# Kernel optimization log

Measured on AMD Instinct MI355X. Metric: run time of the kernel, lower is better.

## Reference

```python
import jax, jax.numpy as jnp
import numpy as np


def setup_inputs() -> dict:
    key = jax.random.key(0)
    ks = jax.random.split(key, 9)
    D, DK, DV = 512, 64, 64
    B, S = 4, 4096
    sd = 1.0 / np.sqrt(D).astype(np.float32)
    so = 1.0 / np.sqrt(DV).astype(np.float32)
    return {
        "x": jax.random.normal(ks[0], (B, S, D), dtype=jnp.float32),
        "Wq": jax.random.normal(ks[1], (D, DK), dtype=jnp.float32) * sd,
        "bq": jnp.zeros((DK,), dtype=jnp.float32),
        "Wk": jax.random.normal(ks[2], (D, DK), dtype=jnp.float32) * sd,
        "bk": jnp.zeros((DK,), dtype=jnp.float32),
        "Wv": jax.random.normal(ks[3], (D, DV), dtype=jnp.float32) * sd,
        "bv": jnp.zeros((DV,), dtype=jnp.float32),
        "Wo": jax.random.normal(ks[4], (DV, D), dtype=jnp.float32) * so,
        "bo": jnp.zeros((D,), dtype=jnp.float32),
    }


def reference(x, Wq, bq, Wk, bk, Wv, bv, Wo, bo):
    # x: (B, S, D)
    B, S, D = x.shape
    dk = Wq.shape[1]
    q = x @ Wq + bq            # (B, S, dk)
    k = x @ Wk + bk            # (B, S, dk)
    v = x @ Wv + bv            # (B, S, dv)
    scores = jnp.einsum("bik,bjk->bij", q, k) / jnp.sqrt(jnp.float32(dk))  # (B,S,S)
    # causal mask: True where j <= i (keep)
    causal = jnp.tril(jnp.ones((S, S), dtype=bool))
    scores = jnp.where(causal[None, :, :], scores, -jnp.inf)
    weights = jax.nn.softmax(scores, axis=-1)   # every row has >=1 unmasked entry
    out = jnp.einsum("bij,bjv->biv", weights, v)  # (B, S, dv)
    return out @ Wo + bo
```

## Files before the change

kernel.cpp:

```cpp
#include <hip/hip_runtime.h>
#include <hip/hip_bf16.h>

#define S_LEN 4096
#define D_MODEL 512
#define DKV 64
#define B_N 4
#define STR 72
#define VSTR 136

typedef __hip_bfloat16 bf16;
typedef __attribute__((ext_vector_type(8))) short short8;
typedef __attribute__((ext_vector_type(4))) float floatx4;

#define MFMA(a, b, c) __builtin_amdgcn_mfma_f32_16x16x32_bf16(a, b, c, 0, 0, 0)

__device__ __forceinline__ float b2f(bf16 v) { return __bfloat162float(v); }

__device__ __forceinline__ unsigned short f2bits(float v) {
    union { bf16 h; unsigned short u; } cv;
    cv.h = __float2bfloat16(v);
    return cv.u;
}
__device__ __forceinline__ float bits2f(unsigned short u) {
    union { bf16 h; unsigned short u; } cv;
    cv.u = u;
    return b2f(cv.h);
}

__global__ __launch_bounds__(64) void detect_kernel(const void* x, int* flag) {
    const int lane = threadIdx.x;
    const bf16* xb = (const bf16*)x;
    int bad = 0;
    for (int k = lane; k < 4096; k += 64) {
        float v = fabsf(b2f(xb[2 * k]));
        if (!(v < 64.f)) bad++;
    }
    #pragma unroll
    for (int off = 32; off >= 1; off >>= 1) bad += __shfl_xor(bad, off);
    if (lane == 0) *flag = (bad > 100) ? 1 : 0;
}

__global__ __launch_bounds__(512) void wprep_qkv_frag(
    const void* __restrict__ Wq, const void* __restrict__ bq,
    const void* __restrict__ Wk, const void* __restrict__ bk,
    const void* __restrict__ Wv, const void* __restrict__ bv,
    bf16* __restrict__ Wfh, bf16* __restrict__ Wfl, float* __restrict__ ball,
    const int* __restrict__ flag)
{
    __shared__ float xs[16][513];
    const int ct = blockIdx.x;
    const int c0 = ct * 16;
    const int g = c0 >> 6;
    const int cc0 = c0 & 63;
    const void* W    = (g == 0) ? Wq : (g == 1) ? Wk : Wv;
    const void* bias = (g == 0) ? bq : (g == 1) ? bk : bv;
    const int tid = threadIdx.x;
    const int f32 = *flag;

    #pragma unroll
    for (int i = 0; i < 16; ++i) {
        const int idx = tid + 512 * i;
        const int d = idx >> 4, j = idx & 15;
        const float v = f32 ? ((const float*)W)[(size_t)d * DKV + cc0 + j]
                            : b2f(((const bf16*)W)[(size_t)d * DKV + cc0 + j]);
        xs[j][d] = v;
    }
    __syncthreads();

    union Pack8 { uint4 u; unsigned short s[8]; };
    #pragma unroll
    for (int rep = 0; rep < 2; ++rep) {
        const int f = tid + rep * 512;
        const int kt = f >> 6, lane = f & 63;
        const int quad = lane >> 4, l15 = lane & 15;
        Pack8 ph, pl;
        #pragma unroll
        for (int j = 0; j < 8; ++j) {
            const float v = xs[l15][kt * 32 + quad * 8 + j];
            const unsigned short hb = f2bits(v);
            ph.s[j] = hb;
            pl.s[j] = f2bits(v - bits2f(hb));
        }
        const size_t o = (((size_t)ct * 16 + kt) * 64 + lane) * 8;
        *(uint4*)&Wfh[o] = ph.u;
        *(uint4*)&Wfl[o] = pl.u;
    }
    if (tid < 16)
        ball[c0 + tid] = f32 ? ((const float*)bias)[cc0 + tid]
                             : b2f(((const bf16*)bias)[cc0 + tid]);
}

__global__ __launch_bounds__(512) void wprep_o_frag(
    const void* __restrict__ Wo, const void* __restrict__ bo,
    bf16* __restrict__ WoFh, bf16* __restrict__ WoFl,
    float* __restrict__ ball2, const int* __restrict__ flag)
{
    __shared__ float ys[16][65];
    const int ctile = blockIdx.x;
    const int c0 = ctile * 16;
    const int tid = threadIdx.x;
    const int f32 = *flag;

    #pragma unroll
    for (int rep = 0; rep < 2; ++rep) {
        const int idx = tid + rep * 512;
        const int d = idx >> 4, j = idx & 15;
        const float v = f32 ? ((const float*)Wo)[(size_t)d * D_MODEL + c0 + j]
                            : b2f(((const bf16*)Wo)[(size_t)d * D_MODEL + c0 + j]);
        ys[j][d] = v;
    }
    __syncthreads();

    union Pack8 { uint4 u; unsigned short s[8]; };
    if (tid < 128) {
        const int kc = tid >> 6, lane = tid & 63;
        const int quad = lane >> 4, l15 = lane & 15;
        Pack8 ph, pl;
        #pragma unroll
        for (int j = 0; j < 8; ++j) {
            const float v = ys[l15][kc * 32 + quad * 8 + j];
            const unsigned short hb = f2bits(v);
            ph.s[j] = hb;
            pl.s[j] = f2bits(v - bits2f(hb));
        }
        const size_t o = (((size_t)ctile * 2 + kc) * 64 + lane) * 8;
        *(uint4*)&WoFh[o] = ph.u;
        *(uint4*)&WoFl[o] = pl.u;
    }
    if (tid < 16)
        ball2[c0 + tid] = f32 ? ((const float*)bo)[c0 + tid]
                              : b2f(((const bf16*)bo)[c0 + tid]);
}

__global__ __launch_bounds__(256) void qkv_mfma_bf16(
    const void* __restrict__ x,
    const bf16* __restrict__ Wfh, const float* __restrict__ ball,
    bf16* __restrict__ Qb, bf16* __restrict__ Kb, bf16* __restrict__ Vt,
    const int* __restrict__ flag)
{
    if (*flag) return;
    __shared__ unsigned short hiA[32 * D_MODEL];
    const int tid = threadIdx.x;
    const int rowBase = blockIdx.x * 32;

    const unsigned short* xr = (const unsigned short*)x + (size_t)rowBase * D_MODEL;
    #pragma unroll
    for (int i = 0; i < 8; ++i) {
        const int idx = tid + 256 * i;
        const int r = idx >> 6;
        const int c0 = (idx & 63) << 3;
        const uint4 hv = *(const uint4*)&xr[r * D_MODEL + c0];
        const int boff = (c0 * 2) ^ ((r & 7) << 4);
        *(uint4*)((char*)hiA + r * 1024 + boff) = hv;
    }
    __syncthreads();

    const int lane = tid & 63;
    const int w    = tid >> 6;
    const int quad = lane >> 4;
    const int l15  = lane & 15;
    const int wr   = w & 1;
    const int wcol = w >> 1;
    const int arow = wr * 16 + l15;
    const char* hib = (const char*)hiA + arow * 1024;
    const int swz = (arow & 7) << 4;

    floatx4 acc[6];
    #pragma unroll
    for (int ct = 0; ct < 6; ++ct) acc[ct] = (floatx4){0.f, 0.f, 0.f, 0.f};

    for (int kt = 0; kt < 16; ++kt) {
        const int boff = (kt * 64 + quad * 16) ^ swz;
        const short8 ah = *(const short8*)(hib + boff);
        #pragma unroll
        for (int ct = 0; ct < 6; ++ct) {
            const size_t fo = (((size_t)(wcol * 6 + ct) * 16 + kt) * 64 + lane) * 8;
            const short8 bh = *(const short8*)&Wfh[fo];
            acc[ct] = MFMA(ah, bh, acc[ct]);
        }
    }

    #pragma unroll
    for (int ct = 0; ct < 6; ++ct) {
        const int gc = wcol * 96 + ct * 16 + l15;
        const float bias = ball[gc];
        const float scale = (gc < 64) ? 0.18033688f : 1.0f;
        #pragma unroll
        for (int r = 0; r < 4; ++r) {
            const int gr = rowBase + wr * 16 + quad * 4 + r;
            const bf16 o = __float2bfloat16((acc[ct][r] + bias) * scale);
            if (gc < 64)       Qb[(size_t)gr * DKV + gc] = o;
            else if (gc < 128) Kb[(size_t)gr * DKV + (gc - 64)] = o;
            else {
                const int bb = gr >> 12, sidx = gr & (S_LEN - 1);
                Vt[((size_t)bb * DKV + (gc - 128)) * S_LEN + sidx] = o;
            }
        }
    }
}

__global__ __launch_bounds__(512) void qkv_mfma_f32(
    const void* __restrict__ x,
    const bf16* __restrict__ Wfh, const bf16* __restrict__ Wfl,
    const float* __restrict__ ball,
    bf16* __restrict__ Qb, bf16* __restrict__ Kb, bf16* __restrict__ Vt,
    const int* __restrict__ flag)
{
    if (!*flag) return;
    __shared__ unsigned short hiA[32 * D_MODEL];
    __shared__ unsigned short loA[32 * D_MODEL];
    const int tid = threadIdx.x;
    const int rowBase = blockIdx.x * 32;

    union Pack8 { uint4 u; unsigned short s[8]; };
    {
        const float* xr = (const float*)x + (size_t)rowBase * D_MODEL;
        #pragma unroll
        for (int i = 0; i < 4; ++i) {
            const int idx = tid + 512 * i;
            const int r = idx >> 6;
            const int c0 = (idx & 63) << 3;
            const float4 v0 = *(const float4*)&xr[r * D_MODEL + c0];
            const float4 v1 = *(const float4*)&xr[r * D_MODEL + c0 + 4];
            const float vv[8] = {v0.x, v0.y, v0.z, v0.w, v1.x, v1.y, v1.z, v1.w};
            Pack8 ph, pl;
            #pragma unroll
            for (int j = 0; j < 8; ++j) {
                const unsigned short hb = f2bits(vv[j]);
                ph.s[j] = hb;
                pl.s[j] = f2bits(vv[j] - bits2f(hb));
            }
            const int boff = (c0 * 2) ^ ((r & 7) << 4);
            *(uint4*)((char*)hiA + r * 1024 + boff) = ph.u;
            *(uint4*)((char*)loA + r * 1024 + boff) = pl.u;
        }
    }
    __syncthreads();

    const int lane = tid & 63;
    const int w    = tid >> 6;
    const int quad = lane >> 4;
    const int l15  = lane & 15;
    const int wr   = w & 1;
    const int wq   = w >> 1;
    const int arow = wr * 16 + l15;
    const char* hib = (const char*)hiA + arow * 1024;
    const char* lob = (const char*)loA + arow * 1024;
    const int swz = (arow & 7) << 4;

    floatx4 acc[3];
    #pragma unroll
    for (int ct = 0; ct < 3; ++ct) acc[ct] = (floatx4){0.f, 0.f, 0.f, 0.f};

    for (int kt = 0; kt < 16; ++kt) {
        const int boff = (kt * 64 + quad * 16) ^ swz;
        const short8 ah = *(const short8*)(hib + boff);
        const short8 al = *(const short8*)(lob + boff);
        #pragma unroll
        for (int ct = 0; ct < 3; ++ct) {
            const size_t fo = (((size_t)(wq * 3 + ct) * 16 + kt) * 64 + lane) * 8;
            const short8 bh = *(const short8*)&Wfh[fo];
            const short8 bl = *(const short8*)&Wfl[fo];
            acc[ct] = MFMA(ah, bh, acc[ct]);
            acc[ct] = MFMA(ah, bl, acc[ct]);
            acc[ct] = MFMA(al, bh, acc[ct]);
        }
    }

    #pragma unroll
    for (int ct = 0; ct < 3; ++ct) {
        const int gc = wq * 48 + ct * 16 + l15;
        const float bias = ball[gc];
        const float scale = (gc < 64) ? 0.18033688f : 1.0f;
        #pragma unroll
        for (int r = 0; r < 4; ++r) {
            const int gr = rowBase + wr * 16 + quad * 4 + r;
            const bf16 o = __float2bfloat16((acc[ct][r] + bias) * scale);
            if (gc < 64)       Qb[(size_t)gr * DKV + gc] = o;
            else if (gc < 128) Kb[(size_t)gr * DKV + (gc - 64)] = o;
            else {
                const int bb = gr >> 12, sidx = gr & (S_LEN - 1);
                Vt[((size_t)bb * DKV + (gc - 128)) * S_LEN + sidx] = o;
            }
        }
    }
}

__global__ __launch_bounds__(256, 3) void attn_mfma(
    const bf16* __restrict__ Qg, const bf16* __restrict__ Kg,
    const bf16* __restrict__ Vtg, float* __restrict__ Op,
    float* __restrict__ Mp, float* __restrict__ Lp, const int NS)
{
    const int bid = blockIdx.x;
    const int xcd = bid & 7;
    const int rest = bid >> 3;
    const int b   = xcd >> 1;
    const int khH = (NS == 4) ? (rest & 1) : 0;
    const int t64 = 63 - ((NS == 4) ? (rest >> 1) : rest);
    const int kh  = khH * 2 + (xcd & 1);
    const int rowBase = t64 * 64;
    const int tid = threadIdx.x;
    const int lane = tid & 63;
    const int w  = tid >> 6;
    const int quad = lane >> 4;
    const int l15  = lane & 15;

    __shared__ bf16 Kl[128 * STR];
    __shared__ bf16 Vl[64 * VSTR];
    __shared__ bf16 Pl[64 * VSTR];

    const bf16* Qb = Qg + ((size_t)b * S_LEN + rowBase) * DKV;
    const bf16* Kb = Kg + (size_t)b * S_LEN * DKV;
    const bf16* Vb = Vtg + (size_t)b * DKV * S_LEN;

    {
        const int qr = tid >> 2, qd = (tid & 3) * 16;
        *(uint4*)&Pl[qr * VSTR + qd]     = *(const uint4*)&Qb[qr * DKV + qd];
        *(uint4*)&Pl[qr * VSTR + qd + 8] = *(const uint4*)&Qb[qr * DKV + qd + 8];
    }
    __syncthreads();
    short8 qf0, qf1;
    {
        const int qoff = (w * 16 + l15) * VSTR + quad * 8;
        qf0 = *(const short8*)&Pl[qoff];
        qf1 = *(const short8*)&Pl[qoff + 32];
    }

    floatx4 acc[4];
    #pragma unroll
    for (int v = 0; v < 4; ++v) acc[v] = (floatx4){0.f, 0.f, 0.f, 0.f};
    float m_run[4], l_run[4];
    #pragma unroll
    for (int r = 0; r < 4; ++r) { m_run[r] = -1e30f; l_run[r] = 0.f; }

    const int kbMax = (rowBase + 63) >> 7;
    const int kk = tid >> 1, dk = (tid & 1) * 32;
    const int vd = tid >> 2, vk = (tid & 3) * 32;

    uint4 kr0, kr1, kr2, kr3, vr0, vr1, vr2, vr3;
    int kb = kh;
    if (kb <= kbMax) {
        const uint4* ks = (const uint4*)&Kb[((size_t)(kb * 128 + kk)) * DKV + dk];
        kr0 = ks[0]; kr1 = ks[1]; kr2 = ks[2]; kr3 = ks[3];
        const uint4* vs = (const uint4*)&Vb[(size_t)vd * S_LEN + kb * 128 + vk];
        vr0 = vs[0]; vr1 = vs[1]; vr2 = vs[2]; vr3 = vs[3];
    }

    for (; kb <= kbMax; kb += NS) {
        __syncthreads();
        {
            uint4* kd = (uint4*)&Kl[kk * STR + dk];
            kd[0] = kr0; kd[1] = kr1; kd[2] = kr2; kd[3] = kr3;
            uint4* vdst = (uint4*)&Vl[vd * VSTR + vk];
            vdst[0] = vr0; vdst[1] = vr1; vdst[2] = vr2; vdst[3] = vr3;
        }
        __syncthreads();
        if (kb + NS <= kbMax) {
            const uint4* ks = (const uint4*)&Kb[((size_t)((kb + NS) * 128 + kk)) * DKV + dk];
            kr0 = ks[0]; kr1 = ks[1]; kr2 = ks[2]; kr3 = ks[3];
            const uint4* vs = (const uint4*)&Vb[(size_t)vd * S_LEN + (kb + NS) * 128 + vk];
            vr0 = vs[0]; vr1 = vs[1]; vr2 = vs[2]; vr3 = vs[3];
        }

        floatx4 s[8];
        #pragma unroll
        for (int jt = 0; jt < 8; ++jt) s[jt] = (floatx4){0.f, 0.f, 0.f, 0.f};
        {
            const int qk = quad * 8;
            #pragma unroll
            for (int jt = 0; jt < 8; ++jt) {
                const int kc = (jt * 16 + l15) * STR + qk;
                const short8 ba = *(const short8*)&Kl[kc];
                const short8 bb = *(const short8*)&Kl[kc + 32];
                s[jt] = MFMA(qf0, ba, s[jt]);
                s[jt] = MFMA(qf1, bb, s[jt]);
            }
        }
        if (kb == kbMax) {
            const int rowg = rowBase + w * 16 + quad * 4;
            #pragma unroll
            for (int jt = 0; jt < 8; ++jt) {
                const int kg = kb * 128 + jt * 16 + l15;
                #pragma unroll
                for (int r = 0; r < 4; ++r)
                    if (kg > rowg + r) s[jt][r] = -1e30f;
            }
        }
        float m4[4];
        #pragma unroll
        for (int r = 0; r < 4; ++r) {
            float mm = s[0][r];
            #pragma unroll
            for (int jt = 1; jt < 8; ++jt) mm = fmaxf(mm, s[jt][r]);
            m4[r] = mm;
        }
        #pragma unroll
        for (int off = 1; off < 16; off <<= 1) {
            #pragma unroll
            for (int r = 0; r < 4; ++r) m4[r] = fmaxf(m4[r], __shfl_xor(m4[r], off));
        }
        float alpha[4];
        #pragma unroll
        for (int r = 0; r < 4; ++r) {
            const float mnew = fmaxf(m_run[r], m4[r]);
            alpha[r] = exp2f(m_run[r] - mnew);
            m_run[r] = mnew;
        }
        float ps[4];
        #pragma unroll
        for (int r = 0; r < 4; ++r) {
            float acc_ps = 0.f;
            #pragma unroll
            for (int jt = 0; jt < 8; ++jt) {
                const float pp = exp2f(s[jt][r] - m_run[r]);
                s[jt][r] = pp;
                acc_ps += pp;
            }
            ps[r] = acc_ps;
        }
        #pragma unroll
        for (int off = 1; off < 16; off <<= 1) {
            #pragma unroll
            for (int r = 0; r < 4; ++r) ps[r] += __shfl_xor(ps[r], off);
        }
        #pragma unroll
        for (int r = 0; r < 4; ++r) {
            l_run[r] = l_run[r] * alpha[r] + ps[r];
            #pragma unroll
            for (int v = 0; v < 4; ++v) acc[v][r] *= alpha[r];
            const int poff = (w * 16 + quad * 4 + r) * VSTR + l15;
            #pragma unroll
            for (int jt = 0; jt < 8; ++jt)
                Pl[poff + jt * 16] = __float2bfloat16(s[jt][r]);
        }
        asm volatile("s_waitcnt lgkmcnt(0)" ::: "memory");

        {
            const int pk = quad * 8;
            const int prow = (w * 16 + l15) * VSTR;
            short8 pa[4];
            #pragma unroll
            for (int c = 0; c < 4; ++c)
                pa[c] = *(const short8*)&Pl[prow + pk + c * 32];
            #pragma unroll
            for (int v = 0; v < 4; ++v) {
                const int vrow = (v * 16 + l15) * VSTR;
                #pragma unroll
                for (int c = 0; c < 4; ++c) {
                    const short8 vb = *(const short8*)&Vl[vrow + pk + c * 32];
                    acc[v] = MFMA(pa[c], vb, acc[v]);
                }
            }
        }
    }
    #pragma unroll
    for (int r = 0; r < 4; ++r) {
        const int row = rowBase + w * 16 + quad * 4 + r;
        float* op = Op + (((size_t)kh * B_N + b) * S_LEN + row) * DKV + l15;
        #pragma unroll
        for (int v = 0; v < 4; ++v) op[v * 16] = acc[v][r];
    }
    if (l15 == 0) {
        #pragma unroll
        for (int r = 0; r < 4; ++r) {
            const int row = rowBase + w * 16 + quad * 4 + r;
            const size_t mi = ((size_t)kh * B_N + b) * S_LEN + row;
            Mp[mi] = m_run[r];
            Lp[mi] = l_run[r];
        }
    }
}

__global__ __launch_bounds__(256) void merge_kernel(
    const float* __restrict__ Op, const float* __restrict__ Mp,
    const float* __restrict__ Lp, bf16* __restrict__ Oh, bf16* __restrict__ Ol,
    const int NS)
{
    const int row = blockIdx.x * 32 + (threadIdx.x >> 3);
    const int d0 = (threadIdx.x & 7) * 8;
    const size_t part = (size_t)B_N * S_LEN;

    float m = -1e30f;
    #pragma unroll 4
    for (int i = 0; i < NS; ++i) m = fmaxf(m, Mp[i * part + row]);

    float oacc[8];
    #pragma unroll
    for (int jj = 0; jj < 8; ++jj) oacc[jj] = 0.f;
    float denom = 0.f;
    #pragma unroll 4
    for (int i = 0; i < NS; ++i) {
        const float wi = exp2f(Mp[i * part + row] - m);
        denom += Lp[i * part + row] * wi;
        const float* pi = Op + (i * part + row) * DKV + d0;
        #pragma unroll
        for (int jj = 0; jj < 8; ++jj) oacc[jj] += pi[jj] * wi;
    }
    const float inv = 1.0f / denom;

    union Pack8 { uint4 u; unsigned short s[8]; };
    Pack8 ph, pl;
    #pragma unroll
    for (int jj = 0; jj < 8; ++jj) {
        const float o = oacc[jj] * inv;
        const unsigned short hb = f2bits(o);
        ph.s[jj] = hb;
        pl.s[jj] = f2bits(o - bits2f(hb));
    }
    *(uint4*)&Oh[(size_t)row * DKV + d0] = ph.u;
    *(uint4*)&Ol[(size_t)row * DKV + d0] = pl.u;
}

#define PSTR 72
__global__ __launch_bounds__(256) void proj_mfma_bf16(
    const bf16* __restrict__ Oh, const bf16* __restrict__ Ol,
    const bf16* __restrict__ WoFh, const float* __restrict__ ball2,
    bf16* __restrict__ out, const int* __restrict__ flag)
{
    if (*flag) return;
    __shared__ unsigned short Ah[32 * PSTR], Al[32 * PSTR];
    const int tid = threadIdx.x;
    const int rowBase = blockIdx.x * 32;

    {
        const int r = tid >> 3, c0 = (tid & 7) * 8;
        *(uint4*)&Ah[r * PSTR + c0] = *(const uint4*)&Oh[(size_t)(rowBase + r) * DKV + c0];
        *(uint4*)&Al[r * PSTR + c0] = *(const uint4*)&Ol[(size_t)(rowBase + r) * DKV + c0];
    }
    __syncthreads();

    const int lane = tid & 63;
    const int w    = tid >> 6;
    const int quad = lane >> 4;
    const int l15  = lane & 15;
    const int wr   = w & 1;
    const int wcq  = w >> 1;

    const int aoff = (wr * 16 + l15) * PSTR + quad * 8;
    const short8 ah0 = *(const short8*)&Ah[aoff];
    const short8 ah1 = *(const short8*)&Ah[aoff + 32];
    const short8 al0 = *(const short8*)&Al[aoff];
    const short8 al1 = *(const short8*)&Al[aoff + 32];

    floatx4 acc[16];
    #pragma unroll
    for (int ct = 0; ct < 16; ++ct) acc[ct] = (floatx4){0.f, 0.f, 0.f, 0.f};

    #pragma unroll
    for (int ct = 0; ct < 16; ++ct) {
        const int ctile = wcq * 16 + ct;
        const size_t o0 = (((size_t)ctile * 2 + 0) * 64 + lane) * 8;
        const size_t o1 = (((size_t)ctile * 2 + 1) * 64 + lane) * 8;
        const short8 bh0 = *(const short8*)&WoFh[o0];
        const short8 bh1 = *(const short8*)&WoFh[o1];
        acc[ct] = MFMA(ah0, bh0, acc[ct]);
        acc[ct] = MFMA(ah1, bh1, acc[ct]);
        acc[ct] = MFMA(al0, bh0, acc[ct]);
        acc[ct] = MFMA(al1, bh1, acc[ct]);
    }

    #pragma unroll
    for (int ct = 0; ct < 16; ++ct) {
        const int col = wcq * 256 + ct * 16 + l15;
        const float bias = ball2[col];
        #pragma unroll
        for (int r = 0; r < 4; ++r) {
            const int row = rowBase + wr * 16 + quad * 4 + r;
            out[(size_t)row * D_MODEL + col] = __float2bfloat16(acc[ct][r] + bias);
        }
    }
}

__global__ __launch_bounds__(512) void proj_mfma_f32(
    const bf16* __restrict__ Oh, const bf16* __restrict__ Ol,
    const bf16* __restrict__ WoFh, const bf16* __restrict__ WoFl,
    const float* __restrict__ ball2, float* __restrict__ out,
    const int* __restrict__ flag)
{
    if (!*flag) return;
    __shared__ unsigned short Ah[32 * PSTR], Al[32 * PSTR];
    const int tid = threadIdx.x;
    const int rowBase = blockIdx.x * 32;

    {
        const int r = (tid & 255) >> 3, c0 = (tid & 7) * 8;
        if (tid < 256)
            *(uint4*)&Ah[r * PSTR + c0] = *(const uint4*)&Oh[(size_t)(rowBase + r) * DKV + c0];
        else
            *(uint4*)&Al[r * PSTR + c0] = *(const uint4*)&Ol[(size_t)(rowBase + r) * DKV + c0];
    }
    __syncthreads();

    const int lane = tid & 63;
    const int w    = tid >> 6;
    const int quad = lane >> 4;
    const int l15  = lane & 15;
    const int wr   = w & 1;
    const int wcq  = w >> 1;

    const int aoff = (wr * 16 + l15) * PSTR + quad * 8;
    const short8 ah0 = *(const short8*)&Ah[aoff];
    const short8 ah1 = *(const short8*)&Ah[aoff + 32];
    const short8 al0 = *(const short8*)&Al[aoff];
    const short8 al1 = *(const short8*)&Al[aoff + 32];

    floatx4 acc[8];
    #pragma unroll
    for (int ct = 0; ct < 8; ++ct) acc[ct] = (floatx4){0.f, 0.f, 0.f, 0.f};

    #pragma unroll
    for (int ct = 0; ct < 8; ++ct) {
        const int ctile = wcq * 8 + ct;
        const size_t o0 = (((size_t)ctile * 2 + 0) * 64 + lane) * 8;
        const size_t o1 = (((size_t)ctile * 2 + 1) * 64 + lane) * 8;
        const short8 bh0 = *(const short8*)&WoFh[o0];
        const short8 bh1 = *(const short8*)&WoFh[o1];
        const short8 bl0 = *(const short8*)&WoFl[o0];
        const short8 bl1 = *(const short8*)&WoFl[o1];
        acc[ct] = MFMA(ah0, bh0, acc[ct]);
        acc[ct] = MFMA(ah1, bh1, acc[ct]);
        acc[ct] = MFMA(ah0, bl0, acc[ct]);
        acc[ct] = MFMA(ah1, bl1, acc[ct]);
        acc[ct] = MFMA(al0, bh0, acc[ct]);
        acc[ct] = MFMA(al1, bh1, acc[ct]);
    }

    #pragma unroll
    for (int ct = 0; ct < 8; ++ct) {
        const int col = wcq * 128 + ct * 16 + l15;
        const float bias = ball2[col];
        #pragma unroll
        for (int r = 0; r < 4; ++r) {
            const int row = rowBase + wr * 16 + quad * 4 + r;
            out[(size_t)row * D_MODEL + col] = acc[ct][r] + bias;
        }
    }
}

extern "C" void kernel_launch(void* const* d_in, const int* in_sizes, int n_in,
                              void* d_out, int out_size, void* d_ws, size_t ws_size,
                              hipStream_t stream) {
    const void* x  = d_in[0];
    const void* Wq = d_in[1];
    const void* bq = d_in[2];
    const void* Wk = d_in[3];
    const void* bk = d_in[4];
    const void* Wv = d_in[5];
    const void* bv = d_in[6];
    const void* Wo = d_in[7];
    const void* bo = d_in[8];

    const int rows = B_N * S_LEN;
    const int NS = (ws_size >= (size_t)30 * 1024 * 1024) ? 4 : 2;

    char* p = (char*)d_ws;
    int*  flag = (int*)p;                          p += 256;
    bf16* Qb = (bf16*)p;                           p += (size_t)rows * DKV * 2;
    bf16* Kb = (bf16*)p;                           p += (size_t)rows * DKV * 2;
    bf16* Vt = (bf16*)p;                           p += (size_t)rows * DKV * 2;
    bf16* Wfh = (bf16*)p;                          p += (size_t)12 * 16 * 64 * 8 * 2;
    bf16* Wfl = (bf16*)p;                          p += (size_t)12 * 16 * 64 * 8 * 2;
    float* ball = (float*)p;                       p += 1024;
    bf16* WoFh = (bf16*)p;                         p += (size_t)32 * 2 * 64 * 8 * 2;
    bf16* WoFl = (bf16*)p;                         p += (size_t)32 * 2 * 64 * 8 * 2;
    float* ball2 = (float*)p;                      p += D_MODEL * 4;
    float* Op = (float*)p;                         p += (size_t)NS * rows * DKV * 4;
    float* Mp = (float*)p;                         p += (size_t)NS * rows * 4;
    float* Lp = (float*)p;                         p += (size_t)NS * rows * 4;
    bf16* Ohb = (bf16*)p;                          p += (size_t)rows * DKV * 2;
    bf16* Olb = (bf16*)p;                          p += (size_t)rows * DKV * 2;

    detect_kernel<<<1, 64, 0, stream>>>(x, flag);
    wprep_qkv_frag<<<12, 512, 0, stream>>>(Wq, bq, Wk, bk, Wv, bv, Wfh, Wfl, ball, flag);
    wprep_o_frag<<<32, 512, 0, stream>>>(Wo, bo, WoFh, WoFl, ball2, flag);
    qkv_mfma_bf16<<<512, 256, 0, stream>>>(x, Wfh, ball, Qb, Kb, Vt, flag);
    qkv_mfma_f32<<<512, 512, 0, stream>>>(x, Wfh, Wfl, ball, Qb, Kb, Vt, flag);
    attn_mfma<<<256 * NS, 256, 0, stream>>>(Qb, Kb, Vt, Op, Mp, Lp, NS);
    merge_kernel<<<512, 256, 0, stream>>>(Op, Mp, Lp, Ohb, Olb, NS);
    proj_mfma_bf16<<<512, 256, 0, stream>>>(Ohb, Olb, WoFh, ball2, (bf16*)d_out, flag);
    proj_mfma_f32<<<512, 512, 0, stream>>>(Ohb, Olb, WoFh, WoFl, ball2, (float*)d_out, flag);
}
```

Measured before the change: 181.9 us.

## Compute softmax row sums via MFMA and fuse split-K merge into output projection

The attention kernel no longer sums the exponentials with per-row loops and cross-lane shuffles. It accumulates the row sum l with extra MFMAs against a ones vector, using the bf16 P values that feed the PV product. The separate merge kernel is removed, and each projection kernel now combines the split partials (Op, Mp, Lp) itself before its MFMAs. This drops one launch and the Oh/Ol bf16 round trip through global memory. The cost is four extra MFMAs per tile, and the denominator is now summed from bf16-rounded probabilities rather than fp32 ones.

```diff
diff --git a/kernel.cpp b/kernel.cpp
--- a/kernel.cpp
+++ b/kernel.cpp
@@ -326,12 +326,16 @@
         qf1 = *(const short8*)&Pl[qoff + 32];
     }
 
+    const short s1b = (short)0x3F80;
+    const short8 ones = {s1b, s1b, s1b, s1b, s1b, s1b, s1b, s1b};
+
     floatx4 acc[4];
     #pragma unroll
     for (int v = 0; v < 4; ++v) acc[v] = (floatx4){0.f, 0.f, 0.f, 0.f};
-    float m_run[4], l_run[4];
-    #pragma unroll
-    for (int r = 0; r < 4; ++r) { m_run[r] = -1e30f; l_run[r] = 0.f; }
+    floatx4 accl = {0.f, 0.f, 0.f, 0.f};
+    float m_run[4];
+    #pragma unroll
+    for (int r = 0; r < 4; ++r) m_run[r] = -1e30f;
 
     const int kbMax = (rowBase + 63) >> 7;
     const int kk = tid >> 1, dk = (tid & 1) * 32;
@@ -406,32 +410,17 @@
             alpha[r] = exp2f(m_run[r] - mnew);
             m_run[r] = mnew;
         }
-        float ps[4];
-        #pragma unroll
-        for (int r = 0; r < 4; ++r) {
-            float acc_ps = 0.f;
+        #pragma unroll
+        for (int r = 0; r < 4; ++r) {
+            accl[r] *= alpha[r];
+            #pragma unroll
+            for (int v = 0; v < 4; ++v) acc[v][r] *= alpha[r];
+            const int poff = (w * 16 + quad * 4 + r) * VSTR + l15;
             #pragma unroll
             for (int jt = 0; jt < 8; ++jt) {
                 const float pp = exp2f(s[jt][r] - m_run[r]);
-                s[jt][r] = pp;
-                acc_ps += pp;
+                Pl[poff + jt * 16] = __float2bfloat16(pp);
             }
-            ps[r] = acc_ps;
-        }
-        #pragma unroll
-        for (int off = 1; off < 16; off <<= 1) {
-            #pragma unroll
-            for (int r = 0; r < 4; ++r) ps[r] += __shfl_xor(ps[r], off);
-        }
-        #pragma unroll
-        for (int r = 0; r < 4; ++r) {
-            l_run[r] = l_run[r] * alpha[r] + ps[r];
-            #pragma unroll
-            for (int v = 0; v < 4; ++v) acc[v][r] *= alpha[r];
-            const int poff = (w * 16 + quad * 4 + r) * VSTR + l15;
-            #pragma unroll
-            for (int jt = 0; jt < 8; ++jt)
-                Pl[poff + jt * 16] = __float2bfloat16(s[jt][r]);
         }
         asm volatile("s_waitcnt lgkmcnt(0)" ::: "memory");
 
@@ -442,6 +431,8 @@
             #pragma unroll
             for (int c = 0; c < 4; ++c)
                 pa[c] = *(const short8*)&Pl[prow + pk + c * 32];
+            #pragma unroll
+            for (int c = 0; c < 4; ++c) accl = MFMA(pa[c], ones, accl);
             #pragma unroll
             for (int v = 0; v < 4; ++v) {
                 const int vrow = (v * 16 + l15) * VSTR;
@@ -466,54 +457,15 @@
             const int row = rowBase + w * 16 + quad * 4 + r;
             const size_t mi = ((size_t)kh * B_N + b) * S_LEN + row;
             Mp[mi] = m_run[r];
-            Lp[mi] = l_run[r];
-        }
-    }
-}
-
-__global__ __launch_bounds__(256) void merge_kernel(
-    const float* __restrict__ Op, const float* __restrict__ Mp,
-    const float* __restrict__ Lp, bf16* __restrict__ Oh, bf16* __restrict__ Ol,
-    const int NS)
-{
-    const int row = blockIdx.x * 32 + (threadIdx.x >> 3);
-    const int d0 = (threadIdx.x & 7) * 8;
-    const size_t part = (size_t)B_N * S_LEN;
-
-    float m = -1e30f;
-    #pragma unroll 4
-    for (int i = 0; i < NS; ++i) m = fmaxf(m, Mp[i * part + row]);
-
-    float oacc[8];
-    #pragma unroll
-    for (int jj = 0; jj < 8; ++jj) oacc[jj] = 0.f;
-    float denom = 0.f;
-    #pragma unroll 4
-    for (int i = 0; i < NS; ++i) {
-        const float wi = exp2f(Mp[i * part + row] - m);
-        denom += Lp[i * part + row] * wi;
-        const float* pi = Op + (i * part + row) * DKV + d0;
-        #pragma unroll
-        for (int jj = 0; jj < 8; ++jj) oacc[jj] += pi[jj] * wi;
-    }
-    const float inv = 1.0f / denom;
-
-    union Pack8 { uint4 u; unsigned short s[8]; };
-    Pack8 ph, pl;
-    #pragma unroll
-    for (int jj = 0; jj < 8; ++jj) {
-        const float o = oacc[jj] * inv;
-        const unsigned short hb = f2bits(o);
-        ph.s[jj] = hb;
-        pl.s[jj] = f2bits(o - bits2f(hb));
-    }
-    *(uint4*)&Oh[(size_t)row * DKV + d0] = ph.u;
-    *(uint4*)&Ol[(size_t)row * DKV + d0] = pl.u;
+            Lp[mi] = accl[r];
+        }
+    }
 }
 
 #define PSTR 72
 __global__ __launch_bounds__(256) void proj_mfma_bf16(
-    const bf16* __restrict__ Oh, const bf16* __restrict__ Ol,
+    const float* __restrict__ Op, const float* __restrict__ Mp,
+    const float* __restrict__ Lp, const int NS,
     const bf16* __restrict__ WoFh, const float* __restrict__ ball2,
     bf16* __restrict__ out, const int* __restrict__ flag)
 {
@@ -523,9 +475,33 @@
     const int rowBase = blockIdx.x * 32;
 
     {
-        const int r = tid >> 3, c0 = (tid & 7) * 8;
-        *(uint4*)&Ah[r * PSTR + c0] = *(const uint4*)&Oh[(size_t)(rowBase + r) * DKV + c0];
-        *(uint4*)&Al[r * PSTR + c0] = *(const uint4*)&Ol[(size_t)(rowBase + r) * DKV + c0];
+        const int rr = tid >> 3, dd = (tid & 7) * 8;
+        const int row = rowBase + rr;
+        const size_t part = (size_t)B_N * S_LEN;
+        float m = -1e30f;
+        #pragma unroll 4
+        for (int i = 0; i < NS; ++i) m = fmaxf(m, Mp[i * part + row]);
+        float denom = 0.f;
+        float oacc[8] = {0.f, 0.f, 0.f, 0.f, 0.f, 0.f, 0.f, 0.f};
+        #pragma unroll 4
+        for (int i = 0; i < NS; ++i) {
+            const float wi = exp2f(Mp[i * part + row] - m);
+            denom += Lp[i * part + row] * wi;
+            const float* pi = Op + (i * part + row) * DKV + dd;
+            #pragma unroll
+            for (int j = 0; j < 8; ++j) oacc[j] += pi[j] * wi;
+        }
+        const float inv = 1.0f / denom;
+        union Pack8 { uint4 u; unsigned short s[8]; };
+        Pack8 ph, pl;
+        #pragma unroll
+        for (int j = 0; j < 8; ++j) {
+            const float o = oacc[j] * inv;
+            ph.s[j] = f2bits(o);
+            pl.s[j] = f2bits(o - bits2f(ph.s[j]));
+        }
+        *(uint4*)&Ah[rr * PSTR + dd] = ph.u;
+        *(uint4*)&Al[rr * PSTR + dd] = pl.u;
     }
     __syncthreads();
 
@@ -572,7 +548,8 @@
 }
 
 __global__ __launch_bounds__(512) void proj_mfma_f32(
-    const bf16* __restrict__ Oh, const bf16* __restrict__ Ol,
+    const float* __restrict__ Op, const float* __restrict__ Mp,
+    const float* __restrict__ Lp, const int NS,
     const bf16* __restrict__ WoFh, const bf16* __restrict__ WoFl,
     const float* __restrict__ ball2, float* __restrict__ out,
     const int* __restrict__ flag)
@@ -583,11 +560,33 @@
     const int rowBase = blockIdx.x * 32;
 
     {
-        const int r = (tid & 255) >> 3, c0 = (tid & 7) * 8;
-        if (tid < 256)
-            *(uint4*)&Ah[r * PSTR + c0] = *(const uint4*)&Oh[(size_t)(rowBase + r) * DKV + c0];
-        else
-            *(uint4*)&Al[r * PSTR + c0] = *(const uint4*)&Ol[(size_t)(rowBase + r) * DKV + c0];
+        const int rr = tid >> 4, dd = (tid & 15) * 4;
+        const int row = rowBase + rr;
+        const size_t part = (size_t)B_N * S_LEN;
+        float m = -1e30f;
+        #pragma unroll 4
+        for (int i = 0; i < NS; ++i) m = fmaxf(m, Mp[i * part + row]);
+        float denom = 0.f;
+        float oacc[4] = {0.f, 0.f, 0.f, 0.f};
+        #pragma unroll 4
+        for (int i = 0; i < NS; ++i) {
+            const float wi = exp2f(Mp[i * part + row] - m);
+            denom += Lp[i * part + row] * wi;
+            const float4 v = *(const float4*)&Op[(i * part + row) * DKV + dd];
+            oacc[0] += v.x * wi; oacc[1] += v.y * wi;
+            oacc[2] += v.z * wi; oacc[3] += v.w * wi;
+        }
+        const float inv = 1.0f / denom;
+        union Pack4 { uint2 u; unsigned short s[4]; };
+        Pack4 ph, pl;
+        #pragma unroll
+        for (int j = 0; j < 4; ++j) {
+            const float o = oacc[j] * inv;
+            ph.s[j] = f2bits(o);
+            pl.s[j] = f2bits(o - bits2f(ph.s[j]));
+        }
+        *(uint2*)&Ah[rr * PSTR + dd] = ph.u;
+        *(uint2*)&Al[rr * PSTR + dd] = pl.u;
     }
     __syncthreads();
 
@@ -667,8 +666,6 @@
     float* Op = (float*)p;                         p += (size_t)NS * rows * DKV * 4;
     float* Mp = (float*)p;                         p += (size_t)NS * rows * 4;
     float* Lp = (float*)p;                         p += (size_t)NS * rows * 4;
-    bf16* Ohb = (bf16*)p;                          p += (size_t)rows * DKV * 2;
-    bf16* Olb = (bf16*)p;                          p += (size_t)rows * DKV * 2;
 
     detect_kernel<<<1, 64, 0, stream>>>(x, flag);
     wprep_qkv_frag<<<12, 512, 0, stream>>>(Wq, bq, Wk, bk, Wv, bv, Wfh, Wfl, ball, flag);
@@ -676,7 +673,6 @@
     qkv_mfma_bf16<<<512, 256, 0, stream>>>(x, Wfh, ball, Qb, Kb, Vt, flag);
     qkv_mfma_f32<<<512, 512, 0, stream>>>(x, Wfh, Wfl, ball, Qb, Kb, Vt, flag);
     attn_mfma<<<256 * NS, 256, 0, stream>>>(Qb, Kb, Vt, Op, Mp, Lp, NS);
-    merge_kernel<<<512, 256, 0, stream>>>(Op, Mp, Lp, Ohb, Olb, NS);
-    proj_mfma_bf16<<<512, 256, 0, stream>>>(Ohb, Olb, WoFh, ball2, (bf16*)d_out, flag);
-    proj_mfma_f32<<<512, 512, 0, stream>>>(Ohb, Olb, WoFh, WoFl, ball2, (float*)d_out, flag);
-}
+    proj_mfma_bf16<<<512, 256, 0, stream>>>(Op, Mp, Lp, NS, WoFh, ball2, (bf16*)d_out, flag);
+    proj_mfma_f32<<<512, 512, 0, stream>>>(Op, Mp, Lp, NS, WoFh, WoFl, ball2, (float*)d_out, flag);
+}
```

New measurement: 173.0 us. 1.05x faster.
